# Optimization experiments

Hardware: AMD Instinct MI355X
Metric: run time of the kernel (lower is better)

The kernel has to match this reference:

```python
import jax, jax.numpy as jnp
import numpy as np

B, C, F = 4, 3, 5
HO, WO = 256, 256
HI, WI = HO + F - 1, WO + F - 1


def setup_inputs() -> dict:
    key = jax.random.key(0)
    k = jax.random.split(key, 6)
    return {
        "tensorInput": jax.random.normal(k[0], (B, C, HI, WI), dtype=jnp.float32),
        "tensorVertical": jax.random.uniform(k[1], (B, F, HO, WO), dtype=jnp.float32),
        "tensorHorizontal": jax.random.uniform(k[2], (B, F, HO, WO), dtype=jnp.float32),
        "tensorOffsetX": jax.random.normal(k[3], (B, F * F, HO, WO), dtype=jnp.float32),
        "tensorOffsetY": jax.random.normal(k[4], (B, F * F, HO, WO), dtype=jnp.float32),
        "tensorMask": jax.random.uniform(k[5], (B, F * F, HO, WO), dtype=jnp.float32),
    }


def _dsepconv(inp, vertical, horizontal, offset_x, offset_y, mask):
    b, c, hin, win = inp.shape
    f = vertical.shape[1]
    ho, wo = vertical.shape[2], vertical.shape[3]
    half = (f - 1) / 2.0

    fy = jnp.arange(f, dtype=inp.dtype).reshape(f, 1, 1, 1)
    fx = jnp.arange(f, dtype=inp.dtype).reshape(1, f, 1, 1)
    hg = jnp.arange(ho, dtype=inp.dtype).reshape(1, 1, ho, 1)
    wg = jnp.arange(wo, dtype=inp.dtype).reshape(1, 1, 1, wo)

    off_y = offset_y.reshape(b, f, f, ho, wo)  # note: code uses offset_y for delta_x
    off_x = offset_x.reshape(b, f, f, ho, wo)  # and offset_x for delta_y

    # sample positions per tap, [B,F,F,Ho,Wo]
    px = jnp.clip(off_y + wg + fx - half + 1.0, 0.0, win - 1)
    py = jnp.clip(off_x + hg + fy - half + 1.0, 0.0, hin - 1)

    left_f = jnp.floor(px)
    top_f = jnp.floor(py)
    wx = 1.0 - (px - left_f)  # bilinear weights
    wy = 1.0 - (py - top_f)

    l = left_f.astype(jnp.int32)
    t = top_f.astype(jnp.int32)
    r = jnp.minimum(l + 1, win - 1)
    btm = jnp.minimum(t + 1, hin - 1)

    def gather(img, yi, xi):
        return img[:, yi, xi]

    g = jax.vmap(gather)
    v_tl = g(inp, t, l)
    v_tr = g(inp, t, r)
    v_bl = g(inp, btm, l)
    v_br = g(inp, btm, r)

    wx_ = wx[:, None]  # add channel axis -> [B,1,F,F,Ho,Wo]
    wy_ = wy[:, None]
    val = (v_tl * wx_ * wy_ + v_tr * (1 - wx_) * wy_
           + v_bl * wx_ * (1 - wy_) + v_br * (1 - wx_) * (1 - wy_))

    # separable filter x mask per tap: [B,F,F,Ho,Wo]
    w_tap = vertical[:, :, None] * horizontal[:, None, :] * mask.reshape(b, f, f, ho, wo)
    # accumulate over the F*F taps
    return jnp.sum(val * w_tap[:, None], axis=(2, 3))  # [B,C,Ho,Wo]


def reference(tensorInput, tensorVertical, tensorHorizontal, tensorOffsetX, tensorOffsetY, tensorMask):
    return _dsepconv(tensorInput, tensorVertical, tensorHorizontal,
                     tensorOffsetX, tensorOffsetY, tensorMask)
```

## Files before the change

kernel.cpp:

```cpp
#include <hip/hip_runtime.h>
#include <hip/hip_fp16.h>

constexpr int B  = 4;
constexpr int C  = 3;
constexpr int F  = 5;
constexpr int HO = 256;
constexpr int WO = 256;
constexpr int HI = HO + F - 1;
constexpr int WI = WO + F - 1;
constexpr int P  = HO * WO;
constexpr int FF = F * F;
constexpr int PI = HI * WI;

constexpr int TROWS = 21;
constexpr int TCOLS = 80;
constexpr int TSTRIDE = 81;
constexpr int TN = TROWS * TCOLS;
constexpr int AMAX = (TROWS - 2) * TSTRIDE + (TCOLS - 2);

__device__ __forceinline__ uint2 pack3(float a, float b, float c) {
    __half2 ab = __floats2half2_rn(a, b);
    __half2 cz = __floats2half2_rn(c, 0.0f);
    uint2 r;
    r.x = *reinterpret_cast<const unsigned int*>(&ab);
    r.y = *reinterpret_cast<const unsigned int*>(&cz);
    return r;
}

__device__ __forceinline__ void fmacc(uint2 v, float w,
                                      float& a0, float& a1, float& a2) {
    __half2 ab = *reinterpret_cast<const __half2*>(&v.x);
    __half2 cz = *reinterpret_cast<const __half2*>(&v.y);
    a0 += __half2float(__low2half(ab))  * w;
    a1 += __half2float(__high2half(ab)) * w;
    a2 += __half2float(__low2half(cz))  * w;
}

__global__ __launch_bounds__(512, 8) void dsepconv_kernel(
    const float* __restrict__ inp,
    const float* __restrict__ vert,
    const float* __restrict__ horz,
    const float* __restrict__ offX,
    const float* __restrict__ offY,
    const float* __restrict__ mask,
    float* __restrict__ out)
{
    __shared__ uint2 tileq[TROWS * TSTRIDE];
    __shared__ float red[4][3][64];

    const int tid  = threadIdx.x;
    const int lane = tid & 63;
    const int wave = tid >> 6;
    const int wrow = wave >> 1;
    const int half = wave & 1;

    const int bx   = blockIdx.x;
    const int x0   = (bx & 3) * 64;
    const int y0   = ((bx >> 2) & 63) * 4;
    const int b    = bx >> 8;

    const float* in0 = inp + (size_t)b * C * PI;
    const float* in1 = in0 + PI;
    const float* in2 = in1 + PI;

    const int ry0 = y0 - 7;
    const int cx0 = x0 - 7;
#pragma unroll 1
    for (int e = tid; e < TN; e += 512) {
        int trow = e / TCOLS;
        int tcol = e - trow * TCOLS;
        int gy = min(max(ry0 + trow, 0), HI - 1);
        int gx = min(max(cx0 + tcol, 0), WI - 1);
        int g = gy * WI + gx;
        tileq[trow * TSTRIDE + tcol] = pack3(in0[g], in1[g], in2[g]);
    }
    __syncthreads();

    const int x   = x0 + lane;
    const int y   = y0 + wrow;
    const int pix = y * WO + x;

    const float* offXb = offX + (size_t)b * FF * P + pix;
    const float* offYb = offY + (size_t)b * FF * P + pix;
    const float* maskb = mask + (size_t)b * FF * P + pix;
    const float* vb    = vert + (size_t)b * F * P + pix;
    const float* hb    = horz + (size_t)b * F * P + pix;

    float acc0 = 0.f, acc1 = 0.f, acc2 = 0.f;

    const int k0 = half ? 12 : 0;
    const int k1 = half ? 25 : 12;

#pragma unroll 1
    for (int k = k0; k < k1; ++k) {
        const int i = k / F;
        const int j = k - i * F;

        float oy = offYb[k * P];
        float ox = offXb[k * P];
        float m  = maskb[k * P];
        float h  = hb[j * P];
        float v  = vb[i * P];

        float px = fminf(fmaxf(oy + (float)(x + j - 1), 0.0f), (float)(WI - 1));
        float py = fminf(fmaxf(ox + (float)(y + i - 1), 0.0f), (float)(HI - 1));

        float lf = floorf(px);
        float tf = floorf(py);
        int l = (int)lf;
        int t = (int)tf;
        float wx = 1.0f - (px - lf);
        float wy = 1.0f - (py - tf);

        float w   = v * h * m;
        float wyw = wy * w;
        float wbw = w - wyw;
        float wtl = wx * wyw;
        float wtr = wyw - wtl;
        float wbl = wx * wbw;
        float wbr = wbw - wbl;

        int lt = t - ry0;
        int ll = l - cx0;
        bool ok = ((unsigned)lt <= TROWS - 2) & ((unsigned)ll <= TCOLS - 2);

        int a = min(max(lt * TSTRIDE + ll, 0), AMAX);

        uint2 g_tl = tileq[a];
        uint2 g_tr = tileq[a + 1];
        uint2 g_bl = tileq[a + TSTRIDE];
        uint2 g_br = tileq[a + TSTRIDE + 1];

        if (__any(!ok)) {
            if (!ok) {
                int r  = min(l + 1, WI - 1);
                int bt = min(t + 1, HI - 1);
                int o_tl = t * WI + l,  o_tr = t * WI + r;
                int o_bl = bt * WI + l, o_br = bt * WI + r;
                g_tl = pack3(in0[o_tl], in1[o_tl], in2[o_tl]);
                g_tr = pack3(in0[o_tr], in1[o_tr], in2[o_tr]);
                g_bl = pack3(in0[o_bl], in1[o_bl], in2[o_bl]);
                g_br = pack3(in0[o_br], in1[o_br], in2[o_br]);
            }
        }

        fmacc(g_tl, wtl, acc0, acc1, acc2);
        fmacc(g_tr, wtr, acc0, acc1, acc2);
        fmacc(g_bl, wbl, acc0, acc1, acc2);
        fmacc(g_br, wbr, acc0, acc1, acc2);
    }

    if (half) {
        red[wrow][0][lane] = acc0;
        red[wrow][1][lane] = acc1;
        red[wrow][2][lane] = acc2;
    }
    __syncthreads();

    if (!half) {
        float* ob = out + (size_t)b * C * P + pix;
        ob[0]     = acc0 + red[wrow][0][lane];
        ob[P]     = acc1 + red[wrow][1][lane];
        ob[2 * P] = acc2 + red[wrow][2][lane];
    }
}

extern "C" void kernel_launch(void* const* d_in, const int* in_sizes, int n_in,
                              void* d_out, int out_size, void* d_ws, size_t ws_size,
                              hipStream_t stream) {
    const float* inp  = (const float*)d_in[0];
    const float* vert = (const float*)d_in[1];
    const float* horz = (const float*)d_in[2];
    const float* offX = (const float*)d_in[3];
    const float* offY = (const float*)d_in[4];
    const float* mask = (const float*)d_in[5];
    float* out = (float*)d_out;

    dim3 block(512);
    dim3 grid(B * (HO / 4) * (WO / 64));
    dsepconv_kernel<<<grid, block, 0, stream>>>(inp, vert, horz, offX, offY, mask, out);
}
```

Before: 26.54 us.

## Prefetch offsets and mask via async global-to-LDS loads in double-buffered batches

Streams offY, offX and mask for each tap into a double-buffered LDS region with global_load_lds, four taps per batch, and issues the first batch before the input tile load. Explicit vmcnt waits let the next batch load while the current one is computed, hiding the latency of the per-tap global reads that previously stalled each loop iteration. This adds 48KB of shared memory per block and lowers the launch-bounds occupancy hint from 8 to 4. The vmcnt counts are hand-tuned and could interact badly with the other global loads in the loop (vert/horz and the fallback path).

```diff
diff --git a/kernel.cpp b/kernel.cpp
--- a/kernel.cpp
+++ b/kernel.cpp
@@ -36,7 +36,7 @@
     a2 += __half2float(__low2half(cz))  * w;
 }
 
-__global__ __launch_bounds__(512, 8) void dsepconv_kernel(
+__global__ __launch_bounds__(512, 4) void dsepconv_kernel(
     const float* __restrict__ inp,
     const float* __restrict__ vert,
     const float* __restrict__ horz,
@@ -45,6 +45,7 @@
     const float* __restrict__ mask,
     float* __restrict__ out)
 {
+    __shared__ float obuf[2][8][4][3][64];
     __shared__ uint2 tileq[TROWS * TSTRIDE];
     __shared__ float red[4][3][64];
 
@@ -62,6 +63,39 @@
     const float* in0 = inp + (size_t)b * C * PI;
     const float* in1 = in0 + PI;
     const float* in2 = in1 + PI;
+
+    const int x   = x0 + lane;
+    const int y   = y0 + wrow;
+    const int pix = y * WO + x;
+
+    const float* offXb = offX + (size_t)b * FF * P + pix;
+    const float* offYb = offY + (size_t)b * FF * P + pix;
+    const float* maskb = mask + (size_t)b * FF * P + pix;
+    const float* vb    = vert + (size_t)b * F * P + pix;
+    const float* hb    = horz + (size_t)b * F * P + pix;
+
+    const int k0 = half ? 12 : 0;
+    const int k1 = half ? 25 : 12;
+    const int NB = half ? 4 : 3;
+    const int k1m1 = k1 - 1;
+
+    auto issue_batch = [&](int bt) {
+        const int kbase = k0 + bt * 4;
+        float* dst = &obuf[bt & 1][wave][0][0][0];
+#pragma unroll
+        for (int t = 0; t < 4; ++t) {
+            int kk = kbase + t;
+            if (kk > k1m1) kk = k1m1;
+            __builtin_amdgcn_global_load_lds(offYb + (size_t)kk * P,
+                                             dst + (t * 3 + 0) * 64, 4, 0, 0);
+            __builtin_amdgcn_global_load_lds(offXb + (size_t)kk * P,
+                                             dst + (t * 3 + 1) * 64, 4, 0, 0);
+            __builtin_amdgcn_global_load_lds(maskb + (size_t)kk * P,
+                                             dst + (t * 3 + 2) * 64, 4, 0, 0);
+        }
+    };
+
+    issue_batch(0);
 
     const int ry0 = y0 - 7;
     const int cx0 = x0 - 7;
@@ -76,78 +110,81 @@
     }
     __syncthreads();
 
-    const int x   = x0 + lane;
-    const int y   = y0 + wrow;
-    const int pix = y * WO + x;
-
-    const float* offXb = offX + (size_t)b * FF * P + pix;
-    const float* offYb = offY + (size_t)b * FF * P + pix;
-    const float* maskb = mask + (size_t)b * FF * P + pix;
-    const float* vb    = vert + (size_t)b * F * P + pix;
-    const float* hb    = horz + (size_t)b * F * P + pix;
-
     float acc0 = 0.f, acc1 = 0.f, acc2 = 0.f;
 
-    const int k0 = half ? 12 : 0;
-    const int k1 = half ? 25 : 12;
-
 #pragma unroll 1
-    for (int k = k0; k < k1; ++k) {
-        const int i = k / F;
-        const int j = k - i * F;
-
-        float oy = offYb[k * P];
-        float ox = offXb[k * P];
-        float m  = maskb[k * P];
-        float h  = hb[j * P];
-        float v  = vb[i * P];
-
-        float px = fminf(fmaxf(oy + (float)(x + j - 1), 0.0f), (float)(WI - 1));
-        float py = fminf(fmaxf(ox + (float)(y + i - 1), 0.0f), (float)(HI - 1));
-
-        float lf = floorf(px);
-        float tf = floorf(py);
-        int l = (int)lf;
-        int t = (int)tf;
-        float wx = 1.0f - (px - lf);
-        float wy = 1.0f - (py - tf);
-
-        float w   = v * h * m;
-        float wyw = wy * w;
-        float wbw = w - wyw;
-        float wtl = wx * wyw;
-        float wtr = wyw - wtl;
-        float wbl = wx * wbw;
-        float wbr = wbw - wbl;
-
-        int lt = t - ry0;
-        int ll = l - cx0;
-        bool ok = ((unsigned)lt <= TROWS - 2) & ((unsigned)ll <= TCOLS - 2);
-
-        int a = min(max(lt * TSTRIDE + ll, 0), AMAX);
-
-        uint2 g_tl = tileq[a];
-        uint2 g_tr = tileq[a + 1];
-        uint2 g_bl = tileq[a + TSTRIDE];
-        uint2 g_br = tileq[a + TSTRIDE + 1];
-
-        if (__any(!ok)) {
-            if (!ok) {
-                int r  = min(l + 1, WI - 1);
-                int bt = min(t + 1, HI - 1);
-                int o_tl = t * WI + l,  o_tr = t * WI + r;
-                int o_bl = bt * WI + l, o_br = bt * WI + r;
-                g_tl = pack3(in0[o_tl], in1[o_tl], in2[o_tl]);
-                g_tr = pack3(in0[o_tr], in1[o_tr], in2[o_tr]);
-                g_bl = pack3(in0[o_bl], in1[o_bl], in2[o_bl]);
-                g_br = pack3(in0[o_br], in1[o_br], in2[o_br]);
+    for (int bt = 0; bt < NB; ++bt) {
+        if (bt + 1 < NB) {
+            issue_batch(bt + 1);
+            asm volatile("s_waitcnt vmcnt(12)" ::: "memory");
+        } else {
+            asm volatile("s_waitcnt vmcnt(0)" ::: "memory");
+        }
+        __builtin_amdgcn_sched_barrier(0);
+
+        const float* cur = &obuf[bt & 1][wave][0][0][0];
+        const int kbase = k0 + bt * 4;
+        const int nt = min(4, k1 - kbase);
+
+#pragma unroll 1
+        for (int t = 0; t < nt; ++t) {
+            const int k = kbase + t;
+            const int i = k / F;
+            const int j = k - i * F;
+
+            float oy = cur[(t * 3 + 0) * 64 + lane];
+            float ox = cur[(t * 3 + 1) * 64 + lane];
+            float m  = cur[(t * 3 + 2) * 64 + lane];
+            float h  = hb[j * P];
+            float v  = vb[i * P];
+
+            float px = fminf(fmaxf(oy + (float)(x + j - 1), 0.0f), (float)(WI - 1));
+            float py = fminf(fmaxf(ox + (float)(y + i - 1), 0.0f), (float)(HI - 1));
+
+            float lf = floorf(px);
+            float tf = floorf(py);
+            int l = (int)lf;
+            int t_ = (int)tf;
+            float wx = 1.0f - (px - lf);
+            float wy = 1.0f - (py - tf);
+
+            float w   = v * h * m;
+            float wyw = wy * w;
+            float wbw = w - wyw;
+            float wtl = wx * wyw;
+            float wtr = wyw - wtl;
+            float wbl = wx * wbw;
+            float wbr = wbw - wbl;
+
+            int lt = t_ - ry0;
+            int ll = l - cx0;
+            bool ok = ((unsigned)lt <= TROWS - 2) & ((unsigned)ll <= TCOLS - 2);
+
+            int a = min(max(lt * TSTRIDE + ll, 0), AMAX);
+
+            uint2 g_tl = tileq[a];
+            uint2 g_tr = tileq[a + 1];
+            uint2 g_bl = tileq[a + TSTRIDE];
+            uint2 g_br = tileq[a + TSTRIDE + 1];
+
+            if (__any(!ok)) {
+                if (!ok) {
+                    int r  = min(l + 1, WI - 1);
+                    int bt_ = min(t_ + 1, HI - 1);
+                    int o_tl = t_ * WI + l,  o_tr = t_ * WI + r;
+                    int o_bl = bt_ * WI + l, o_br = bt_ * WI + r;
+                    g_tl = pack3(in0[o_tl], in1[o_tl], in2[o_tl]);
+                    g_tr = pack3(in0[o_tr], in1[o_tr], in2[o_tr]);
+                    g_bl = pack3(in0[o_bl], in1[o_bl], in2[o_bl]);
+                    g_br = pack3(in0[o_br], in1[o_br], in2[o_br]);
+                }
             }
+
+            fmacc(g_tl, wtl, acc0, acc1, acc2);
+            fmacc(g_tr, wtr, acc0, acc1, acc2);
+            fmacc(g_bl, wbl, acc0, acc1, acc2);
+            fmacc(g_br, wbr, acc0, acc1, acc2);
         }
-
-        fmacc(g_tl, wtl, acc0, acc1, acc2);
-        fmacc(g_tr, wtr, acc0, acc1, acc2);
-        fmacc(g_bl, wbl, acc0, acc1, acc2);
-        fmacc(g_br, wbr, acc0, acc1, acc2);
     }
 
     if (half) {
```

New measurement: 33.00 us. +24.3%, slower.

## Prefetch per-tap offset, mask and filter streams into registers before tile staging

Applied to the files above, without the earlier changes.

All offset, mask and separable-filter values a thread needs are now loaded into register arrays at kernel start, before the shared-memory input tile is filled. The goal is to overlap those global loads with tile staging and the barrier. The tap loop is fully unrolled through templated helpers specialised for each half of the taps, which removes per-iteration index arithmetic. In exchange the register footprint grows, and the launch-bounds occupancy hint is lowered from 8 to 4 to allow for that, which can reduce latency hiding. A stray label placed inside the unrolled loop has no functional effect.

```diff
diff --git a/kernel.cpp b/kernel.cpp
--- a/kernel.cpp
+++ b/kernel.cpp
@@ -36,7 +36,95 @@
     a2 += __half2float(__low2half(cz))  * w;
 }
 
-__global__ __launch_bounds__(512, 8) void dsepconv_kernel(
+template <int K0, int NK>
+__device__ __forceinline__ void load_streams(
+    const float* __restrict__ offYb, const float* __restrict__ offXb,
+    const float* __restrict__ maskb,
+    const float* __restrict__ vb, const float* __restrict__ hb,
+    float (&oy)[13], float (&ox)[13], float (&mk)[13],
+    float (&vv)[3], float (&hh)[5])
+{
+#pragma unroll
+    for (int q = 0; q < NK; ++q) oy[q] = offYb[(K0 + q) * P];
+#pragma unroll
+    for (int q = 0; q < NK; ++q) ox[q] = offXb[(K0 + q) * P];
+#pragma unroll
+    for (int q = 0; q < NK; ++q) mk[q] = maskb[(K0 + q) * P];
+    constexpr int IB = K0 / F;
+#pragma unroll
+    for (int q = 0; q < 3; ++q) vv[q] = vb[(IB + q) * P];
+#pragma unroll
+    for (int q = 0; q < 5; ++q) hh[q] = hb[q * P];
+}
+
+template <int K0, int NK>
+__device__ __forceinline__ void compute_taps(
+    const uint2* __restrict__ tileq,
+    const float* __restrict__ in0, const float* __restrict__ in1,
+    const float* __restrict__ in2,
+    const float (&oy)[13], const float (&ox)[13], const float (&mk)[13],
+    const float (&vv)[3], const float (&hh)[5],
+    int x, int y, int ry0, int cx0,
+    float& acc0, float& acc1, float& acc2)
+{
+    constexpr int IB = K0 / F;
+#pragma unroll
+    for (int q = 0; q < NK; ++q) {
+        constexpr_int:
+        const int k = K0 + q;
+        const int i = k / F;
+        const int j = k % F;
+
+        float px = fminf(fmaxf(oy[q] + (float)(x + j - 1), 0.0f), (float)(WI - 1));
+        float py = fminf(fmaxf(ox[q] + (float)(y + i - 1), 0.0f), (float)(HI - 1));
+
+        float lf = floorf(px);
+        float tf = floorf(py);
+        int l  = (int)lf;
+        int t_ = (int)tf;
+        float wx = 1.0f - (px - lf);
+        float wy = 1.0f - (py - tf);
+
+        float w   = vv[i - IB] * hh[j] * mk[q];
+        float wyw = wy * w;
+        float wbw = w - wyw;
+        float wtl = wx * wyw;
+        float wtr = wyw - wtl;
+        float wbl = wx * wbw;
+        float wbr = wbw - wbl;
+
+        int lt = t_ - ry0;
+        int ll = l - cx0;
+        bool ok = ((unsigned)lt <= TROWS - 2) & ((unsigned)ll <= TCOLS - 2);
+
+        int a = min(max(lt * TSTRIDE + ll, 0), AMAX);
+
+        uint2 g_tl = tileq[a];
+        uint2 g_tr = tileq[a + 1];
+        uint2 g_bl = tileq[a + TSTRIDE];
+        uint2 g_br = tileq[a + TSTRIDE + 1];
+
+        if (__any(!ok)) {
+            if (!ok) {
+                int r  = min(l + 1, WI - 1);
+                int bt = min(t_ + 1, HI - 1);
+                int o_tl = t_ * WI + l,  o_tr = t_ * WI + r;
+                int o_bl = bt * WI + l,  o_br = bt * WI + r;
+                g_tl = pack3(in0[o_tl], in1[o_tl], in2[o_tl]);
+                g_tr = pack3(in0[o_tr], in1[o_tr], in2[o_tr]);
+                g_bl = pack3(in0[o_bl], in1[o_bl], in2[o_bl]);
+                g_br = pack3(in0[o_br], in1[o_br], in2[o_br]);
+            }
+        }
+
+        fmacc(g_tl, wtl, acc0, acc1, acc2);
+        fmacc(g_tr, wtr, acc0, acc1, acc2);
+        fmacc(g_bl, wbl, acc0, acc1, acc2);
+        fmacc(g_br, wbr, acc0, acc1, acc2);
+    }
+}
+
+__global__ __launch_bounds__(512, 4) void dsepconv_kernel(
     const float* __restrict__ inp,
     const float* __restrict__ vert,
     const float* __restrict__ horz,
@@ -63,6 +151,23 @@
     const float* in1 = in0 + PI;
     const float* in2 = in1 + PI;
 
+    const int x   = x0 + lane;
+    const int y   = y0 + wrow;
+    const int pix = y * WO + x;
+
+    const float* offXb = offX + (size_t)b * FF * P + pix;
+    const float* offYb = offY + (size_t)b * FF * P + pix;
+    const float* maskb = mask + (size_t)b * FF * P + pix;
+    const float* vb    = vert + (size_t)b * F * P + pix;
+    const float* hb    = horz + (size_t)b * F * P + pix;
+
+    float oy[13], ox[13], mk[13], vv[3], hh[5];
+    if (half == 0) {
+        load_streams<0, 12>(offYb, offXb, maskb, vb, hb, oy, ox, mk, vv, hh);
+    } else {
+        load_streams<12, 13>(offYb, offXb, maskb, vb, hb, oy, ox, mk, vv, hh);
+    }
+
     const int ry0 = y0 - 7;
     const int cx0 = x0 - 7;
 #pragma unroll 1
@@ -76,78 +181,14 @@
     }
     __syncthreads();
 
-    const int x   = x0 + lane;
-    const int y   = y0 + wrow;
-    const int pix = y * WO + x;
-
-    const float* offXb = offX + (size_t)b * FF * P + pix;
-    const float* offYb = offY + (size_t)b * FF * P + pix;
-    const float* maskb = mask + (size_t)b * FF * P + pix;
-    const float* vb    = vert + (size_t)b * F * P + pix;
-    const float* hb    = horz + (size_t)b * F * P + pix;
-
     float acc0 = 0.f, acc1 = 0.f, acc2 = 0.f;
 
-    const int k0 = half ? 12 : 0;
-    const int k1 = half ? 25 : 12;
-
-#pragma unroll 1
-    for (int k = k0; k < k1; ++k) {
-        const int i = k / F;
-        const int j = k - i * F;
-
-        float oy = offYb[k * P];
-        float ox = offXb[k * P];
-        float m  = maskb[k * P];
-        float h  = hb[j * P];
-        float v  = vb[i * P];
-
-        float px = fminf(fmaxf(oy + (float)(x + j - 1), 0.0f), (float)(WI - 1));
-        float py = fminf(fmaxf(ox + (float)(y + i - 1), 0.0f), (float)(HI - 1));
-
-        float lf = floorf(px);
-        float tf = floorf(py);
-        int l = (int)lf;
-        int t = (int)tf;
-        float wx = 1.0f - (px - lf);
-        float wy = 1.0f - (py - tf);
-
-        float w   = v * h * m;
-        float wyw = wy * w;
-        float wbw = w - wyw;
-        float wtl = wx * wyw;
-        float wtr = wyw - wtl;
-        float wbl = wx * wbw;
-        float wbr = wbw - wbl;
-
-        int lt = t - ry0;
-        int ll = l - cx0;
-        bool ok = ((unsigned)lt <= TROWS - 2) & ((unsigned)ll <= TCOLS - 2);
-
-        int a = min(max(lt * TSTRIDE + ll, 0), AMAX);
-
-        uint2 g_tl = tileq[a];
-        uint2 g_tr = tileq[a + 1];
-        uint2 g_bl = tileq[a + TSTRIDE];
-        uint2 g_br = tileq[a + TSTRIDE + 1];
-
-        if (__any(!ok)) {
-            if (!ok) {
-                int r  = min(l + 1, WI - 1);
-                int bt = min(t + 1, HI - 1);
-                int o_tl = t * WI + l,  o_tr = t * WI + r;
-                int o_bl = bt * WI + l, o_br = bt * WI + r;
-                g_tl = pack3(in0[o_tl], in1[o_tl], in2[o_tl]);
-                g_tr = pack3(in0[o_tr], in1[o_tr], in2[o_tr]);
-                g_bl = pack3(in0[o_bl], in1[o_bl], in2[o_bl]);
-                g_br = pack3(in0[o_br], in1[o_br], in2[o_br]);
-            }
-        }
-
-        fmacc(g_tl, wtl, acc0, acc1, acc2);
-        fmacc(g_tr, wtr, acc0, acc1, acc2);
-        fmacc(g_bl, wbl, acc0, acc1, acc2);
-        fmacc(g_br, wbr, acc0, acc1, acc2);
+    if (half == 0) {
+        compute_taps<0, 12>(tileq, in0, in1, in2, oy, ox, mk, vv, hh,
+                            x, y, ry0, cx0, acc0, acc1, acc2);
+    } else {
+        compute_taps<12, 13>(tileq, in0, in1, in2, oy, ox, mk, vv, hh,
+                             x, y, ry0, cx0, acc0, acc1, acc2);
     }
 
     if (half) {
```

Result: slower. 71.41 us (+169.0%).

## Software-pipeline tap loop with register prefetch and LDS lookahead

Applied to the files above, without the earlier changes.

Restructures the per-tap loop into a two-stage software pipeline: the global loads of offsets, mask and filter values for the next tap are issued before the current tap's LDS gathers, and the accumulate of tap k overlaps the LDS reads of tap k+1. The first tap's global loads are also hoisted above the tile fill and barrier. The tile stride changes from 81 to 85 to alter the LDS bank mapping. This aims to hide global and LDS latency at the cost of more live registers under the 512x8 launch bound, which could cause spilling.

```diff
diff --git a/kernel.cpp b/kernel.cpp
--- a/kernel.cpp
+++ b/kernel.cpp
@@ -14,7 +14,7 @@
 
 constexpr int TROWS = 21;
 constexpr int TCOLS = 80;
-constexpr int TSTRIDE = 81;
+constexpr int TSTRIDE = 85;
 constexpr int TN = TROWS * TCOLS;
 constexpr int AMAX = (TROWS - 2) * TSTRIDE + (TCOLS - 2);
 
@@ -34,6 +34,81 @@
     a0 += __half2float(__low2half(ab))  * w;
     a1 += __half2float(__high2half(ab)) * w;
     a2 += __half2float(__low2half(cz))  * w;
+}
+
+struct Tap {
+    float wx, wy, w;
+    int   l, t;
+    bool  ok;
+    uint2 g0, g1, g2, g3;
+};
+
+__device__ __forceinline__ void loadStreams(
+    int k, const float* __restrict__ offYb, const float* __restrict__ offXb,
+    const float* __restrict__ maskb, const float* __restrict__ vb,
+    const float* __restrict__ hb,
+    float& oy, float& ox, float& m, float& h, float& v)
+{
+    int i = k / F;
+    int j = k - i * F;
+    oy = offYb[(size_t)k * P];
+    ox = offXb[(size_t)k * P];
+    m  = maskb[(size_t)k * P];
+    h  = hb[j * P];
+    v  = vb[i * P];
+}
+
+__device__ __forceinline__ void stageA(
+    int k, Tap& S, float oy, float ox, float m, float h, float v,
+    const uint2* __restrict__ tileq, int x, int y, int ry0, int cx0)
+{
+    int i = k / F;
+    int j = k - i * F;
+    float px = fminf(fmaxf(oy + (float)(x + j - 1), 0.0f), (float)(WI - 1));
+    float py = fminf(fmaxf(ox + (float)(y + i - 1), 0.0f), (float)(HI - 1));
+    float lf = floorf(px);
+    float tf = floorf(py);
+    S.l  = (int)lf;
+    S.t  = (int)tf;
+    S.wx = 1.0f - (px - lf);
+    S.wy = 1.0f - (py - tf);
+    S.w  = v * h * m;
+    int lt = S.t - ry0;
+    int ll = S.l - cx0;
+    S.ok = ((unsigned)lt <= TROWS - 2) & ((unsigned)ll <= TCOLS - 2);
+    int a = min(max(lt * TSTRIDE + ll, 0), AMAX);
+    S.g0 = tileq[a];
+    S.g1 = tileq[a + 1];
+    S.g2 = tileq[a + TSTRIDE];
+    S.g3 = tileq[a + TSTRIDE + 1];
+}
+
+__device__ __forceinline__ void stageB(
+    Tap& S, const float* __restrict__ in0, const float* __restrict__ in1,
+    const float* __restrict__ in2, float& acc0, float& acc1, float& acc2)
+{
+    if (__any(!S.ok)) {
+        if (!S.ok) {
+            int r  = min(S.l + 1, WI - 1);
+            int bt = min(S.t + 1, HI - 1);
+            int o_tl = S.t * WI + S.l, o_tr = S.t * WI + r;
+            int o_bl = bt * WI + S.l,  o_br = bt * WI + r;
+            S.g0 = pack3(in0[o_tl], in1[o_tl], in2[o_tl]);
+            S.g1 = pack3(in0[o_tr], in1[o_tr], in2[o_tr]);
+            S.g2 = pack3(in0[o_bl], in1[o_bl], in2[o_bl]);
+            S.g3 = pack3(in0[o_br], in1[o_br], in2[o_br]);
+        }
+    }
+    float wyw = S.wy * S.w;
+    float wbw = S.w - wyw;
+    float wtl = S.wx * wyw;
+    float wtr = wyw - wtl;
+    float wbl = S.wx * wbw;
+    float wbr = wbw - wbl;
+    fmacc(S.g0, wtl, acc0, acc1, acc2);
+    fmacc(S.g1, wtr, acc0, acc1, acc2);
+    fmacc(S.g2, wbl, acc0, acc1, acc2);
+    fmacc(S.g3, wbr, acc0, acc1, acc2);
 }
 
 __global__ __launch_bounds__(512, 8) void dsepconv_kernel(
@@ -62,6 +137,23 @@
     const float* in0 = inp + (size_t)b * C * PI;
     const float* in1 = in0 + PI;
     const float* in2 = in1 + PI;
+
+    const int x   = x0 + lane;
+    const int y   = y0 + wrow;
+    const int pix = y * WO + x;
+
+    const float* offXb = offX + (size_t)b * FF * P + pix;
+    const float* offYb = offY + (size_t)b * FF * P + pix;
+    const float* maskb = mask + (size_t)b * FF * P + pix;
+    const float* vb    = vert + (size_t)b * F * P + pix;
+    const float* hb    = horz + (size_t)b * F * P + pix;
+
+    const int k0   = half ? 12 : 0;
+    const int k1   = half ? 25 : 12;
+    const int klast = k1 - 1;
+
+    float oy, ox, m, h, v, oy_n, ox_n, m_n, h_n, v_n;
+    loadStreams(k0, offYb, offXb, maskb, vb, hb, oy, ox, m, h, v);
 
     const int ry0 = y0 - 7;
     const int cx0 = x0 - 7;
@@ -76,78 +168,35 @@
     }
     __syncthreads();
 
-    const int x   = x0 + lane;
-    const int y   = y0 + wrow;
-    const int pix = y * WO + x;
-
-    const float* offXb = offX + (size_t)b * FF * P + pix;
-    const float* offYb = offY + (size_t)b * FF * P + pix;
-    const float* maskb = mask + (size_t)b * FF * P + pix;
-    const float* vb    = vert + (size_t)b * F * P + pix;
-    const float* hb    = horz + (size_t)b * F * P + pix;
-
     float acc0 = 0.f, acc1 = 0.f, acc2 = 0.f;
-
-    const int k0 = half ? 12 : 0;
-    const int k1 = half ? 25 : 12;
-
+    Tap SA, SB;
+
+    loadStreams(min(k0 + 1, klast), offYb, offXb, maskb, vb, hb,
+                oy_n, ox_n, m_n, h_n, v_n);
+    stageA(k0, SA, oy, ox, m, h, v, tileq, x, y, ry0, cx0);
+    oy = oy_n; ox = ox_n; m = m_n; h = h_n; v = v_n;
+
+    int k = k0 + 1;
 #pragma unroll 1
-    for (int k = k0; k < k1; ++k) {
-        const int i = k / F;
-        const int j = k - i * F;
-
-        float oy = offYb[k * P];
-        float ox = offXb[k * P];
-        float m  = maskb[k * P];
-        float h  = hb[j * P];
-        float v  = vb[i * P];
-
-        float px = fminf(fmaxf(oy + (float)(x + j - 1), 0.0f), (float)(WI - 1));
-        float py = fminf(fmaxf(ox + (float)(y + i - 1), 0.0f), (float)(HI - 1));
-
-        float lf = floorf(px);
-        float tf = floorf(py);
-        int l = (int)lf;
-        int t = (int)tf;
-        float wx = 1.0f - (px - lf);
-        float wy = 1.0f - (py - tf);
-
-        float w   = v * h * m;
-        float wyw = wy * w;
-        float wbw = w - wyw;
-        float wtl = wx * wyw;
-        float wtr = wyw - wtl;
-        float wbl = wx * wbw;
-        float wbr = wbw - wbl;
-
-        int lt = t - ry0;
-        int ll = l - cx0;
-        bool ok = ((unsigned)lt <= TROWS - 2) & ((unsigned)ll <= TCOLS - 2);
-
-        int a = min(max(lt * TSTRIDE + ll, 0), AMAX);
-
-        uint2 g_tl = tileq[a];
-        uint2 g_tr = tileq[a + 1];
-        uint2 g_bl = tileq[a + TSTRIDE];
-        uint2 g_br = tileq[a + TSTRIDE + 1];
-
-        if (__any(!ok)) {
-            if (!ok) {
-                int r  = min(l + 1, WI - 1);
-                int bt = min(t + 1, HI - 1);
-                int o_tl = t * WI + l,  o_tr = t * WI + r;
-                int o_bl = bt * WI + l, o_br = bt * WI + r;
-                g_tl = pack3(in0[o_tl], in1[o_tl], in2[o_tl]);
-                g_tr = pack3(in0[o_tr], in1[o_tr], in2[o_tr]);
-                g_bl = pack3(in0[o_bl], in1[o_bl], in2[o_bl]);
-                g_br = pack3(in0[o_br], in1[o_br], in2[o_br]);
-            }
-        }
-
-        fmacc(g_tl, wtl, acc0, acc1, acc2);
-        fmacc(g_tr, wtr, acc0, acc1, acc2);
-        fmacc(g_bl, wbl, acc0, acc1, acc2);
-        fmacc(g_br, wbr, acc0, acc1, acc2);
+    for (; k + 1 < k1; k += 2) {
+        loadStreams(min(k + 1, klast), offYb, offXb, maskb, vb, hb,
+                    oy_n, ox_n, m_n, h_n, v_n);
+        stageA(k, SB, oy, ox, m, h, v, tileq, x, y, ry0, cx0);
+        oy = oy_n; ox = ox_n; m = m_n; h = h_n; v = v_n;
+        stageB(SA, in0, in1, in2, acc0, acc1, acc2);
+
+        loadStreams(min(k + 2, klast), offYb, offXb, maskb, vb, hb,
+                    oy_n, ox_n, m_n, h_n, v_n);
+        stageA(k + 1, SA, oy, ox, m, h, v, tileq, x, y, ry0, cx0);
+        oy = oy_n; ox = ox_n; m = m_n; h = h_n; v = v_n;
+        stageB(SB, in0, in1, in2, acc0, acc1, acc2);
+    }
+    if (k < k1) {
+        stageA(k, SB, oy, ox, m, h, v, tileq, x, y, ry0, cx0);
+        stageB(SA, in0, in1, in2, acc0, acc1, acc2);
+        stageB(SB, in0, in1, in2, acc0, acc1, acc2);
+    } else {
+        stageB(SA, in0, in1, in2, acc0, acc1, acc2);
     }
 
     if (half) {
```

Result: slower. 66.61 us (+150.9%).
